# Kernel tuning notes

Measured on AMD Instinct MI355X. Metric: run time of the kernel, lower is better.

The kernel has to match this reference:

```python
import jax, jax.numpy as jnp
import numpy as np

ENTITY_NUM = 500000
RELATION_NUM = 1000
DIM = 256
BATCH = 16384
MARGIN = 1.0
EPS = 1e-6  # torch.nn.PairwiseDistance default eps, added to the difference


def setup_inputs() -> dict:
    key = jax.random.key(0)
    ks = jax.random.split(key, 10)
    entity_emb = jax.random.normal(ks[0], (ENTITY_NUM, DIM), jnp.float32) * 0.1
    entity_map_emb = jax.random.normal(ks[1], (ENTITY_NUM, DIM), jnp.float32) * 0.1
    rel_emb = jax.random.normal(ks[2], (RELATION_NUM, DIM), jnp.float32) * 0.1
    rel_map_emb = jax.random.normal(ks[3], (RELATION_NUM, DIM), jnp.float32) * 0.1

    def make_triples(kh, kr, kt):
        h = jax.random.randint(kh, (BATCH, 1), 0, ENTITY_NUM, jnp.int64)
        r = jax.random.randint(kr, (BATCH, 1), 0, RELATION_NUM, jnp.int64)
        t = jax.random.randint(kt, (BATCH, 1), 0, ENTITY_NUM, jnp.int64)
        return jnp.concatenate([h, r, t], axis=1)

    pos_x = make_triples(ks[4], ks[5], ks[6])
    neg_x = make_triples(ks[7], ks[8], ks[9])
    return {
        "pos_x": pos_x,
        "neg_x": neg_x,
        "entity_emb": entity_emb,
        "entity_map_emb": entity_map_emb,
        "rel_emb": rel_emb,
        "rel_map_emb": rel_map_emb,
    }


def _score(tri, entity_emb, entity_map_emb, rel_emb, rel_map_emb):
    # tri: [B, 3] = (head, relation, tail)
    h_idx, r_idx, t_idx = tri[:, 0], tri[:, 1], tri[:, 2]
    h = entity_emb[h_idx]          # [B, D]
    hp = entity_map_emb[h_idx]     # [B, D]
    t = entity_emb[t_idx]          # [B, D]
    tp = entity_map_emb[t_idx]     # [B, D]
    r = rel_emb[r_idx]             # [B, D]
    rp = rel_map_emb[r_idx]        # [B, D]
    # Mrh = rp hp^T + I  =>  Mrh @ h = rp * (hp . h) + h  (rank-1 update, same math,
    # avoids materializing [B, D, D])
    h_proj = rp * jnp.sum(hp * h, axis=-1, keepdims=True) + h
    t_proj = rp * jnp.sum(tp * t, axis=-1, keepdims=True) + t
    diff = h_proj + r - t_proj + EPS  # PairwiseDistance adds eps to the difference
    return jnp.sqrt(jnp.sum(diff * diff, axis=-1))  # [B]


def reference(pos_x, neg_x, entity_emb, entity_map_emb, rel_emb, rel_map_emb):
    pos_score = _score(pos_x, entity_emb, entity_map_emb, rel_emb, rel_map_emb)
    neg_score = _score(neg_x, entity_emb, entity_map_emb, rel_emb, rel_map_emb)
    b = pos_x.shape[0]
    return jnp.sum(jax.nn.relu(pos_score - neg_score + MARGIN)) / b
```

## Files before the change

kernel.cpp:

```cpp
#include <hip/hip_runtime.h>

#define DIM 256
#define BATCH 16384
#define MARGIN 1.0f
#define EPSV 1e-6f

#define NBLOCKS (BATCH / 2)

typedef float fx4 __attribute__((ext_vector_type(4)));

__device__ __forceinline__ fx4 nt_load4(const void* p) {
    return __builtin_nontemporal_load((const fx4*)p);
}

__device__ __forceinline__ float dot4(fx4 a, fx4 b) {
    return a.x * b.x + a.y * b.y + a.z * b.z + a.w * b.w;
}

__global__ __launch_bounds__(256, 8) void transd_score_kernel(
    const int* __restrict__ pos_x, const int* __restrict__ neg_x,
    const float* __restrict__ ent, const float* __restrict__ entm,
    const float* __restrict__ rel, const float* __restrict__ relm,
    float* __restrict__ partial) {
    const int gwave = (blockIdx.x * blockDim.x + threadIdx.x) >> 6;
    const int lane  = threadIdx.x & 63;
    const int pair  = gwave >> 1;
    const int* __restrict__ tri = (gwave & 1) ? neg_x : pos_x;

    const int h_idx = tri[pair * 3 + 0];
    const int r_idx = tri[pair * 3 + 1];
    const int t_idx = tri[pair * 3 + 2];

    const unsigned lb   = (unsigned)lane << 4;
    const unsigned hoff = ((unsigned)h_idx << 10) + lb;
    const unsigned toff = ((unsigned)t_idx << 10) + lb;
    const unsigned roff = ((unsigned)r_idx << 10) + lb;

    fx4 hv  = nt_load4((const char*)ent  + hoff);
    fx4 hpv = nt_load4((const char*)entm + hoff);
    fx4 tv  = nt_load4((const char*)ent  + toff);
    fx4 tpv = nt_load4((const char*)entm + toff);
    fx4 rv  = *(const fx4*)((const char*)rel  + roff);
    fx4 rpv = *(const fx4*)((const char*)relm + roff);

    float a = dot4(hv, hpv);
    float b = dot4(tv, tpv);
#pragma unroll
    for (int m = 32; m > 0; m >>= 1) {
        a += __shfl_xor(a, m, 64);
        b += __shfl_xor(b, m, 64);
    }
    const float ab = a - b;

    float dx = rpv.x * ab + hv.x + rv.x - tv.x + EPSV;
    float dy = rpv.y * ab + hv.y + rv.y - tv.y + EPSV;
    float dz = rpv.z * ab + hv.z + rv.z - tv.z + EPSV;
    float dw = rpv.w * ab + hv.w + rv.w - tv.w + EPSV;

    float ss = dx * dx + dy * dy + dz * dz + dw * dw;
#pragma unroll
    for (int m = 32; m > 0; m >>= 1) ss += __shfl_xor(ss, m, 64);

    __shared__ float sc[4];
    if (lane == 0) sc[threadIdx.x >> 6] = sqrtf(ss);
    __syncthreads();
    if (threadIdx.x == 0) {
        float va = sc[0] - sc[1] + MARGIN;
        float vb = sc[2] - sc[3] + MARGIN;
        partial[blockIdx.x] = (va > 0.0f ? va : 0.0f) + (vb > 0.0f ? vb : 0.0f);
    }
}

__global__ __launch_bounds__(256) void reduce_kernel(const float* __restrict__ partial,
                                                     float* __restrict__ out) {
    const int lane = threadIdx.x & 63;
    float s = 0.0f;
    for (int i = threadIdx.x; i < NBLOCKS; i += 256) s += partial[i];
#pragma unroll
    for (int m = 32; m > 0; m >>= 1) s += __shfl_xor(s, m, 64);
    __shared__ float smem[4];
    if (lane == 0) smem[threadIdx.x >> 6] = s;
    __syncthreads();
    if (threadIdx.x == 0)
        out[0] = ((smem[0] + smem[1]) + (smem[2] + smem[3])) / (float)BATCH;
}

extern "C" void kernel_launch(void* const* d_in, const int* in_sizes, int n_in,
                              void* d_out, int out_size, void* d_ws, size_t ws_size,
                              hipStream_t stream) {
    const int*   pos_x = (const int*)d_in[0];
    const int*   neg_x = (const int*)d_in[1];
    const float* ent   = (const float*)d_in[2];
    const float* entm  = (const float*)d_in[3];
    const float* rel   = (const float*)d_in[4];
    const float* relm  = (const float*)d_in[5];

    float* partial = (float*)d_ws;
    float* out     = (float*)d_out;

    transd_score_kernel<<<NBLOCKS, 256, 0, stream>>>(pos_x, neg_x, ent, entm, rel, relm, partial);
    reduce_kernel<<<1, 256, 0, stream>>>(partial, out);
}
```

Baseline: 36.94 us.

## Stage gathered embedding rows into LDS via direct global-to-LDS loads, 8 pairs per block

Each block now handles 8 pos/neg pairs instead of 2. Every wave issues 16 direct global_load_lds transfers of entity rows into a 64 KB shared buffer, then reads them back after a barrier. The aim is more memory-level parallelism per wave and fewer register-held loads, so random row gathers overlap better. In exchange the large LDS footprint limits occupancy to about 2 blocks per CU, the nontemporal hints are dropped, and there is an extra LDS round-trip plus a barrier.

Measured after the change: 35.01 us. -5.2%, faster.

```diff
diff --git a/kernel.cpp b/kernel.cpp
--- a/kernel.cpp
+++ b/kernel.cpp
@@ -1,74 +1,122 @@
 #include <hip/hip_runtime.h>
+#include <stdint.h>
 
 #define DIM 256
 #define BATCH 16384
 #define MARGIN 1.0f
 #define EPSV 1e-6f
 
-#define NBLOCKS (BATCH / 2)
+#define PPB 8
+#define NBLOCKS (BATCH / PPB)
 
 typedef float fx4 __attribute__((ext_vector_type(4)));
-
-__device__ __forceinline__ fx4 nt_load4(const void* p) {
-    return __builtin_nontemporal_load((const fx4*)p);
-}
 
 __device__ __forceinline__ float dot4(fx4 a, fx4 b) {
     return a.x * b.x + a.y * b.y + a.z * b.z + a.w * b.w;
 }
 
-__global__ __launch_bounds__(256, 8) void transd_score_kernel(
+__device__ __forceinline__ void gload_lds16(const void* g, void* l) {
+    __builtin_amdgcn_global_load_lds(
+        (const __attribute__((address_space(1))) uint32_t*)g,
+        (__attribute__((address_space(3))) uint32_t*)l, 16, 0, 0);
+}
+
+__global__ __launch_bounds__(256, 2) void transd_loss_kernel(
     const int* __restrict__ pos_x, const int* __restrict__ neg_x,
     const float* __restrict__ ent, const float* __restrict__ entm,
     const float* __restrict__ rel, const float* __restrict__ relm,
     float* __restrict__ partial) {
-    const int gwave = (blockIdx.x * blockDim.x + threadIdx.x) >> 6;
-    const int lane  = threadIdx.x & 63;
-    const int pair  = gwave >> 1;
-    const int* __restrict__ tri = (gwave & 1) ? neg_x : pos_x;
+    __shared__ float rows[64 * DIM];
+    __shared__ float wsum[4];
 
-    const int h_idx = tri[pair * 3 + 0];
-    const int r_idx = tri[pair * 3 + 1];
-    const int t_idx = tri[pair * 3 + 2];
+    const int tid  = threadIdx.x;
+    const int w    = tid >> 6;
+    const int lane = tid & 63;
+    const int g0   = blockIdx.x * PPB;
 
-    const unsigned lb   = (unsigned)lane << 4;
-    const unsigned hoff = ((unsigned)h_idx << 10) + lb;
-    const unsigned toff = ((unsigned)t_idx << 10) + lb;
-    const unsigned roff = ((unsigned)r_idx << 10) + lb;
+    int hidx[2][2], ridx[2][2], tidx[2][2];
+#pragma unroll
+    for (int p2 = 0; p2 < 2; ++p2) {
+        const int p = 2 * w + p2;
+#pragma unroll
+        for (int s = 0; s < 2; ++s) {
+            const int* __restrict__ tri = s ? neg_x : pos_x;
+            hidx[p2][s] = tri[(g0 + p) * 3 + 0];
+            ridx[p2][s] = tri[(g0 + p) * 3 + 1];
+            tidx[p2][s] = tri[(g0 + p) * 3 + 2];
+        }
+    }
 
-    fx4 hv  = nt_load4((const char*)ent  + hoff);
-    fx4 hpv = nt_load4((const char*)entm + hoff);
-    fx4 tv  = nt_load4((const char*)ent  + toff);
-    fx4 tpv = nt_load4((const char*)entm + toff);
-    fx4 rv  = *(const fx4*)((const char*)rel  + roff);
-    fx4 rpv = *(const fx4*)((const char*)relm + roff);
+    const int lf = lane * 4;
+#pragma unroll
+    for (int p2 = 0; p2 < 2; ++p2) {
+        const int p = 2 * w + p2;
+#pragma unroll
+        for (int s = 0; s < 2; ++s) {
+            float* rb = &rows[(p * 8 + s * 4) * DIM];
+            const size_t ho = (size_t)hidx[p2][s] * DIM + lf;
+            const size_t to = (size_t)tidx[p2][s] * DIM + lf;
+            gload_lds16(ent  + ho, rb + 0 * DIM);
+            gload_lds16(entm + ho, rb + 1 * DIM);
+            gload_lds16(ent  + to, rb + 2 * DIM);
+            gload_lds16(entm + to, rb + 3 * DIM);
+        }
+    }
 
-    float a = dot4(hv, hpv);
-    float b = dot4(tv, tpv);
+    fx4 rv[2][2], rpv[2][2];
 #pragma unroll
-    for (int m = 32; m > 0; m >>= 1) {
-        a += __shfl_xor(a, m, 64);
-        b += __shfl_xor(b, m, 64);
+    for (int p2 = 0; p2 < 2; ++p2) {
+#pragma unroll
+        for (int s = 0; s < 2; ++s) {
+            const size_t ro = (size_t)ridx[p2][s] * DIM + lf;
+            rv[p2][s]  = *(const fx4*)(rel  + ro);
+            rpv[p2][s] = *(const fx4*)(relm + ro);
+        }
     }
-    const float ab = a - b;
 
-    float dx = rpv.x * ab + hv.x + rv.x - tv.x + EPSV;
-    float dy = rpv.y * ab + hv.y + rv.y - tv.y + EPSV;
-    float dz = rpv.z * ab + hv.z + rv.z - tv.z + EPSV;
-    float dw = rpv.w * ab + hv.w + rv.w - tv.w + EPSV;
+    __syncthreads();
 
-    float ss = dx * dx + dy * dy + dz * dz + dw * dw;
+    float acc = 0.0f;
 #pragma unroll
-    for (int m = 32; m > 0; m >>= 1) ss += __shfl_xor(ss, m, 64);
+    for (int p2 = 0; p2 < 2; ++p2) {
+        const int p  = 2 * w + p2;
+        const float* rb0 = &rows[(p * 8 + 0) * DIM];
+        const float* rb1 = &rows[(p * 8 + 4) * DIM];
+        fx4 h0  = *(const fx4*)(rb0 + 0 * DIM + lf);
+        fx4 hp0 = *(const fx4*)(rb0 + 1 * DIM + lf);
+        fx4 t0  = *(const fx4*)(rb0 + 2 * DIM + lf);
+        fx4 tp0 = *(const fx4*)(rb0 + 3 * DIM + lf);
+        fx4 h1  = *(const fx4*)(rb1 + 0 * DIM + lf);
+        fx4 hp1 = *(const fx4*)(rb1 + 1 * DIM + lf);
+        fx4 t1  = *(const fx4*)(rb1 + 2 * DIM + lf);
+        fx4 tp1 = *(const fx4*)(rb1 + 3 * DIM + lf);
 
-    __shared__ float sc[4];
-    if (lane == 0) sc[threadIdx.x >> 6] = sqrtf(ss);
+        float a0 = dot4(h0, hp0), b0 = dot4(t0, tp0);
+        float a1 = dot4(h1, hp1), b1 = dot4(t1, tp1);
+#pragma unroll
+        for (int m = 32; m > 0; m >>= 1) {
+            a0 += __shfl_xor(a0, m, 64);
+            b0 += __shfl_xor(b0, m, 64);
+            a1 += __shfl_xor(a1, m, 64);
+            b1 += __shfl_xor(b1, m, 64);
+        }
+        const float ab0 = a0 - b0, ab1 = a1 - b1;
+
+        fx4 d0 = rpv[p2][0] * ab0 + h0 + rv[p2][0] - t0 + EPSV;
+        fx4 d1 = rpv[p2][1] * ab1 + h1 + rv[p2][1] - t1 + EPSV;
+        float ss0 = dot4(d0, d0), ss1 = dot4(d1, d1);
+#pragma unroll
+        for (int m = 32; m > 0; m >>= 1) {
+            ss0 += __shfl_xor(ss0, m, 64);
+            ss1 += __shfl_xor(ss1, m, 64);
+        }
+        const float v = sqrtf(ss0) - sqrtf(ss1) + MARGIN;
+        acc += v > 0.0f ? v : 0.0f;
+    }
+
+    if (lane == 0) wsum[w] = acc;
     __syncthreads();
-    if (threadIdx.x == 0) {
-        float va = sc[0] - sc[1] + MARGIN;
-        float vb = sc[2] - sc[3] + MARGIN;
-        partial[blockIdx.x] = (va > 0.0f ? va : 0.0f) + (vb > 0.0f ? vb : 0.0f);
-    }
+    if (tid == 0) partial[blockIdx.x] = (wsum[0] + wsum[1]) + (wsum[2] + wsum[3]);
 }
 
 __global__ __launch_bounds__(256) void reduce_kernel(const float* __restrict__ partial,
@@ -98,6 +146,6 @@
     float* partial = (float*)d_ws;
     float* out     = (float*)d_out;
 
-    transd_score_kernel<<<NBLOCKS, 256, 0, stream>>>(pos_x, neg_x, ent, entm, rel, relm, partial);
+    transd_loss_kernel<<<NBLOCKS, 256, 0, stream>>>(pos_x, neg_x, ent, entm, rel, relm, partial);
     reduce_kernel<<<1, 256, 0, stream>>>(partial, out);
 }
```
